# Kernel tuning notes

Measured on AMD Instinct MI355X. Metric: run time of the kernel, lower is better.

The kernel has to match this reference:

```python
import jax, jax.numpy as jnp
import numpy as np

N = 100000   # graph nodes
E = 600000   # edges
D = 128      # feature_dim
K = 3        # candidate ops per MixedOp
EPS = 1e-5   # BatchNorm eps


def _param_stack(key, n_ops):
    kW, kb = jax.random.split(key)
    W = jax.random.normal(kW, (n_ops, K, D, D), jnp.float32) * (1.0 / np.sqrt(D))
    b = jax.random.normal(kb, (n_ops, K, D), jnp.float32) * 0.01
    g = jnp.ones((n_ops, K, D), jnp.float32)
    be = jnp.zeros((n_ops, K, D), jnp.float32)
    return W, b, g, be


def setup_inputs() -> dict:
    key = jax.random.key(0)
    ks = jax.random.split(key, 16)
    inp = {
        'src_emb': jax.random.normal(ks[0], (N, D), jnp.float32),
        'hr': jax.random.normal(ks[1], (N, D), jnp.float32),
        'edge_src': jax.random.randint(ks[2], (E,), 0, N),
        'edge_dst': jax.random.randint(ks[3], (E,), 0, N),
        'weights_zero': jax.random.uniform(ks[4], (1, K), jnp.float32),
        'weights_first': jax.random.uniform(ks[5], (3, K), jnp.float32),
        'weights_middle': jax.random.uniform(ks[6], (2, K), jnp.float32),
        'weights_last': jax.random.uniform(ks[7], (2, K), jnp.float32),
    }
    for name, k, n_ops in [('zero', ks[8], 1), ('first', ks[9], 3), ('mid', ks[10], 2), ('last', ks[11], 2)]:
        W, b, g, be = _param_stack(k, n_ops)
        inp[f'W_{name}'] = W; inp[f'b_{name}'] = b
        inp[f'g_{name}'] = g; inp[f'be_{name}'] = be
    inp['W_cat'] = jax.random.normal(ks[12], (3 * D, D), jnp.float32) * (1.0 / np.sqrt(3 * D))
    inp['b_cat'] = jax.random.normal(ks[13], (D,), jnp.float32) * 0.01
    inp['g_cat'] = jnp.ones((D,), jnp.float32)
    inp['be_cat'] = jnp.zeros((D,), jnp.float32)
    return inp


def _mean_agg(h, src, dst):
    s = jax.ops.segment_sum(h[src], dst, num_segments=N)            # [N,D]
    deg = jax.ops.segment_sum(jnp.ones((src.shape[0],), h.dtype), dst, num_segments=N)
    return s / jnp.maximum(deg, 1.0)[:, None]


def _max_agg(h, src, dst):
    m = jax.ops.segment_max(h[src], dst, num_segments=N)            # -inf for empty segs
    return jnp.where(jnp.isfinite(m), m, 0.0)


def _mixed(cands, w, W, b, g, be):
    # cands: list of K [N,D]; w:[K]; W:[K,D,D]; b/g/be:[K,D]
    x = jnp.stack(cands)                                            # [K,N,D]
    y = jnp.einsum('knd,kdf->knf', x, W) + b[:, None, :]            # Linear per candidate
    mu = jnp.mean(y, axis=1, keepdims=True)                         # BatchNorm1d (batch stats)
    var = jnp.var(y, axis=1, keepdims=True)
    y = (y - mu) * jax.lax.rsqrt(var + EPS) * g[:, None, :] + be[:, None, :]
    y = jax.nn.relu(y)
    return jnp.einsum('k,knd->nd', w, y)                            # alpha-weighted sum


def _graph_cands(h, src, dst):
    return [h, _mean_agg(h, src, dst), _max_agg(h, src, dst)]


def _cell_forward(src_emb, hr, edge_src, edge_dst,
                  weights_zero, weights_first, weights_middle, weights_last,
                  W_zero, b_zero, g_zero, be_zero,
                  W_first, b_first, g_first, be_first,
                  W_mid, b_mid, g_mid, be_mid,
                  W_last, b_last, g_last, be_last,
                  W_cat, b_cat, g_cat, be_cat):
    src, dst = edge_src, edge_dst
    # Cell_Zero: relation-composition candidates on (src_emb, hr)
    pre = [src_emb, src_emb - hr, src_emb * hr]
    h_in = _mixed(pre, weights_zero[0], W_zero[0], b_zero[0], g_zero[0], be_zero[0])
    # Cell_First (nodes=2): ops layout [(i=0,j=0),(i=1,j=0),(i=1,j=1)]
    states = [h_in]
    s0 = _mixed(_graph_cands(states[0], src, dst), weights_first[0], W_first[0], b_first[0], g_first[0], be_first[0])
    states.append(s0)
    s1 = (_mixed(_graph_cands(states[0], src, dst), weights_first[1], W_first[1], b_first[1], g_first[1], be_first[1])
          + _mixed(_graph_cands(states[1], src, dst), weights_first[2], W_first[2], b_first[2], g_first[2], be_first[2]))
    states.append(s1)
    states = states[1:]                                             # drop h_in -> len 2
    # Cell_Middle (nodes=2): one MixedOp per state
    states = [_mixed(_graph_cands(states[i], src, dst), weights_middle[i], W_mid[i], b_mid[i], g_mid[i], be_mid[i])
              for i in range(2)]
    # Cell_Last (in_nodes=2, nodes=1): one new state from both inputs; returns all 3
    s_last = (_mixed(_graph_cands(states[0], src, dst), weights_last[0], W_last[0], b_last[0], g_last[0], be_last[0])
              + _mixed(_graph_cands(states[1], src, dst), weights_last[1], W_last[1], b_last[1], g_last[1], be_last[1]))
    states = states + [s_last]                                      # len 3
    # concat -> Linear -> BN -> ReLU (dropout p=0)
    h = jnp.concatenate(states, axis=1) @ W_cat + b_cat             # [N,D]
    mu = jnp.mean(h, axis=0, keepdims=True)
    var = jnp.var(h, axis=0, keepdims=True)
    h = (h - mu) * jax.lax.rsqrt(var + EPS) * g_cat + be_cat
    return jax.nn.relu(h)


def reference(src_emb, hr, edge_src, edge_dst,
              weights_zero, weights_first, weights_middle, weights_last,
              W_zero, b_zero, g_zero, be_zero,
              W_first, b_first, g_first, be_first,
              W_mid, b_mid, g_mid, be_mid,
              W_last, b_last, g_last, be_last,
              W_cat, b_cat, g_cat, be_cat):
    return _cell_forward(src_emb, hr, edge_src, edge_dst,
                         weights_zero, weights_first, weights_middle, weights_last,
                         W_zero, b_zero, g_zero, be_zero,
                         W_first, b_first, g_first, be_first,
                         W_mid, b_mid, g_mid, be_mid,
                         W_last, b_last, g_last, be_last,
                         W_cat, b_cat, g_cat, be_cat)
```

## Files before the change

### kernel.cpp

```cpp
#include <hip/hip_runtime.h>

#define N_NODES 100000
#define N_EDGES 600000
#define NPAD    100096
#define NTILES  782
#define SCAN_B  98
#define EPS_F   1e-5f

typedef __bf16 bf16_t;
typedef __bf16 bf16x8 __attribute__((ext_vector_type(8)));
typedef __bf16 bf16x4 __attribute__((ext_vector_type(4)));
typedef float  f32x4  __attribute__((ext_vector_type(4)));

__global__ __launch_bounds__(256)
void init_zero_kernel(int* __restrict__ deg, float* __restrict__ stats)
{
    int i = blockIdx.x * 256 + threadIdx.x;
    if (i < N_NODES) deg[i] = 0;
    if (i < 9 * 768) stats[i] = 0.f;
}

__global__ __launch_bounds__(256)
void transpose_w_kernel(const float* __restrict__ Wz, const float* __restrict__ Wf,
                        const float* __restrict__ Wm, const float* __restrict__ Wl,
                        const float* __restrict__ Wc, bf16_t* __restrict__ wt)
{
    int idx = blockIdx.x * 256 + threadIdx.x;
    int mat = idx >> 14;
    int off = idx & 16383;
    int n = off >> 7, kk = off & 127;
    const float* src;
    if      (mat < 3)  src = Wz + mat * 16384;
    else if (mat < 12) src = Wf + (mat - 3) * 16384;
    else if (mat < 18) src = Wm + (mat - 12) * 16384;
    else if (mat < 24) src = Wl + (mat - 18) * 16384;
    else               src = Wc + (mat - 24) * 16384;
    wt[idx] = (bf16_t)src[kk * 128 + n];
}

__global__ __launch_bounds__(256)
void pre_kernel(const float* __restrict__ se, const float* __restrict__ hr,
                bf16_t* __restrict__ p0, bf16_t* __restrict__ p1, bf16_t* __restrict__ p2)
{
    long i = ((long)blockIdx.x * 256 + threadIdx.x) * 8;
    float4 a0 = *(const float4*)&se[i], a1 = *(const float4*)&se[i + 4];
    float4 b0 = *(const float4*)&hr[i], b1 = *(const float4*)&hr[i + 4];
    float av[8] = {a0.x, a0.y, a0.z, a0.w, a1.x, a1.y, a1.z, a1.w};
    float bv[8] = {b0.x, b0.y, b0.z, b0.w, b1.x, b1.y, b1.z, b1.w};
    bf16x8 o0, o1, o2;
#pragma unroll
    for (int j = 0; j < 8; ++j) {
        o0[j] = (bf16_t)av[j];
        o1[j] = (bf16_t)(av[j] - bv[j]);
        o2[j] = (bf16_t)(av[j] * bv[j]);
    }
    *(bf16x8*)&p0[i] = o0;
    *(bf16x8*)&p1[i] = o1;
    *(bf16x8*)&p2[i] = o2;
}

__global__ __launch_bounds__(256)
void deg_count_kernel(const int* __restrict__ dst, int* __restrict__ deg)
{
    int i = blockIdx.x * 256 + threadIdx.x;
    if (i < N_EDGES) atomicAdd(&deg[dst[i]], 1);
}

__global__ __launch_bounds__(256)
void scan_a_kernel(const int* __restrict__ deg, int* __restrict__ partials)
{
    __shared__ int ls[256];
    int b = blockIdx.x, t = threadIdx.x;
    int s = 0;
    for (int j = 0; j < 4; ++j) {
        int i = b * 1024 + t * 4 + j;
        if (i < N_NODES) s += deg[i];
    }
    ls[t] = s; __syncthreads();
    for (int o = 128; o > 0; o >>= 1) {
        if (t < o) ls[t] += ls[t + o];
        __syncthreads();
    }
    if (t == 0) partials[b] = ls[0];
}

__global__ void scan_b_kernel(const int* __restrict__ partials, int* __restrict__ pofs)
{
    if (threadIdx.x == 0) {
        int a = 0;
        for (int i = 0; i < SCAN_B; ++i) { pofs[i] = a; a += partials[i]; }
    }
}

__global__ __launch_bounds__(256)
void scan_c_kernel(const int* __restrict__ deg, const int* __restrict__ pofs,
                   int* __restrict__ row_ptr, int* __restrict__ cursor)
{
    __shared__ int ls[256];
    int b = blockIdx.x, t = threadIdx.x;
    int v[4], s = 0;
    for (int j = 0; j < 4; ++j) {
        int i = b * 1024 + t * 4 + j;
        v[j] = (i < N_NODES) ? deg[i] : 0;
        s += v[j];
    }
    ls[t] = s; __syncthreads();
    for (int o = 1; o < 256; o <<= 1) {
        int tv = (t >= o) ? ls[t - o] : 0;
        __syncthreads();
        ls[t] += tv;
        __syncthreads();
    }
    int excl = ls[t] - s + pofs[b];
    for (int j = 0; j < 4; ++j) {
        int i = b * 1024 + t * 4 + j;
        if (i < N_NODES) { row_ptr[i] = excl; cursor[i] = excl; excl += v[j]; }
    }
    if (b == 0 && t == 0) row_ptr[N_NODES] = N_EDGES;
}

__global__ __launch_bounds__(256)
void scatter_kernel(const int* __restrict__ src, const int* __restrict__ dst,
                    int* __restrict__ cursor, int* __restrict__ csr_src)
{
    int i = blockIdx.x * 256 + threadIdx.x;
    if (i < N_EDGES) {
        int p = atomicAdd(&cursor[dst[i]], 1);
        csr_src[p] = src[i];
    }
}

__global__ __launch_bounds__(256)
void agg_kernel(const bf16_t* __restrict__ h, const int* __restrict__ row_ptr,
                const int* __restrict__ csr_src,
                bf16_t* __restrict__ mean_o, bf16_t* __restrict__ max_o)
{
    int node = blockIdx.x * 16 + (threadIdx.x >> 4);
    int dd = (threadIdx.x & 15) * 8;
    int e0 = row_ptr[node], e1 = row_ptr[node + 1];
    float s[8], mx[8];
#pragma unroll
    for (int j = 0; j < 8; ++j) { s[j] = 0.f; mx[j] = 0.f; }
    for (int e = e0; e < e1; ++e) {
        int sc = csr_src[e];
        bf16x8 v = *(const bf16x8*)&h[(long)sc * 128 + dd];
#pragma unroll
        for (int j = 0; j < 8; ++j) {
            float f = (float)v[j];
            s[j] += f;
            mx[j] = fmaxf(mx[j], f);
        }
    }
    float inv = 1.f / fmaxf((float)(e1 - e0), 1.f);
    bf16x8 om, ox;
#pragma unroll
    for (int j = 0; j < 8; ++j) { om[j] = (bf16_t)(s[j] * inv); ox[j] = (bf16_t)mx[j]; }
    *(bf16x8*)&mean_o[(long)node * 128 + dd] = om;
    *(bf16x8*)&max_o [(long)node * 128 + dd] = ox;
}

__global__ __launch_bounds__(256, 2)
void gemm_kernel(const bf16_t* __restrict__ x0, const bf16_t* __restrict__ x1,
                 const bf16_t* __restrict__ x2, const bf16_t* __restrict__ wt,
                 const float* __restrict__ bias, bf16_t* __restrict__ out,
                 float* __restrict__ partial, int mode)
{
    __shared__ bf16_t lds_w[16384];
    __shared__ bf16_t lds_x[16384];
    const int tid  = threadIdx.x;
    const int lane = tid & 63;
    const int wave = tid >> 6;
    const int quad = lane >> 4;
    const int t16  = lane & 15;
    const int wr = wave >> 1, wc = wave & 1;
    const long tile_base = (long)blockIdx.x * 128;

    f32x4 acc[4][4];
#pragma unroll
    for (int a = 0; a < 4; ++a)
#pragma unroll
        for (int b = 0; b < 4; ++b) acc[a][b] = (f32x4){0.f, 0.f, 0.f, 0.f};

    const int k_sel = blockIdx.y;
    const int nchunk = (mode == 0) ? 1 : 3;
    const bf16_t* xk = (k_sel == 0) ? x0 : ((k_sel == 1) ? x1 : x2);
    bf16_t* outp = (mode == 0) ? (out + (long)k_sel * NPAD * 128) : out;
    const float* bp = (mode == 0) ? (bias + k_sel * 128) : bias;

    for (int c3 = 0; c3 < nchunk; ++c3) {
        const bf16_t* xcur = (mode == 0) ? xk : ((c3 == 0) ? x0 : ((c3 == 1) ? x1 : x2));
        const bf16_t* wcur = (mode == 0) ? (wt + k_sel * 16384) : (wt + c3 * 16384);
        if (c3) __syncthreads();
#pragma unroll
        for (int i = 0; i < 8; ++i) {
            int idx = tid + i * 256;
            int row = idx >> 4, c = idx & 15;
            int sw = c ^ (row & 15);
            *(uint4*)&lds_w[row * 128 + sw * 8] = *(const uint4*)&wcur[row * 128 + c * 8];
            *(uint4*)&lds_x[row * 128 + sw * 8] = *(const uint4*)&xcur[(tile_base + row) * 128 + c * 8];
        }
        __syncthreads();
#pragma unroll
        for (int ks = 0; ks < 4; ++ks) {
            bf16x8 xf[4], wf[4];
#pragma unroll
            for (int ms = 0; ms < 4; ++ms) {
                int row = wr * 64 + ms * 16 + t16;
                int sw = (ks * 4 + quad) ^ t16;
                xf[ms] = *(const bf16x8*)&lds_x[row * 128 + sw * 8];
            }
#pragma unroll
            for (int ns = 0; ns < 4; ++ns) {
                int row = wc * 64 + ns * 16 + t16;
                int sw = (ks * 4 + quad) ^ t16;
                wf[ns] = *(const bf16x8*)&lds_w[row * 128 + sw * 8];
            }
#pragma unroll
            for (int ns = 0; ns < 4; ++ns)
#pragma unroll
                for (int ms = 0; ms < 4; ++ms)
                    acc[ns][ms] = __builtin_amdgcn_mfma_f32_16x16x32_bf16(
                        wf[ns], xf[ms], acc[ns][ms], 0, 0, 0);
        }
    }

    float ss[16], sq[16];
#pragma unroll
    for (int i = 0; i < 16; ++i) { ss[i] = 0.f; sq[i] = 0.f; }

#pragma unroll
    for (int ms = 0; ms < 4; ++ms) {
        long m = tile_base + wr * 64 + ms * 16 + t16;
        if (m < N_NODES) {
#pragma unroll
            for (int ns = 0; ns < 4; ++ns) {
                int n0 = wc * 64 + ns * 16 + quad * 4;
                float4 b4 = *(const float4*)&bp[n0];
                float v0 = acc[ns][ms][0] + b4.x;
                float v1 = acc[ns][ms][1] + b4.y;
                float v2 = acc[ns][ms][2] + b4.z;
                float v3 = acc[ns][ms][3] + b4.w;
                ss[ns * 4 + 0] += v0; sq[ns * 4 + 0] += v0 * v0;
                ss[ns * 4 + 1] += v1; sq[ns * 4 + 1] += v1 * v1;
                ss[ns * 4 + 2] += v2; sq[ns * 4 + 2] += v2 * v2;
                ss[ns * 4 + 3] += v3; sq[ns * 4 + 3] += v3 * v3;
                bf16x4 ov;
                ov[0] = (bf16_t)v0; ov[1] = (bf16_t)v1;
                ov[2] = (bf16_t)v2; ov[3] = (bf16_t)v3;
                *(bf16x4*)&outp[m * 128 + n0] = ov;
            }
        }
    }

#pragma unroll
    for (int o = 1; o < 16; o <<= 1) {
#pragma unroll
        for (int i = 0; i < 16; ++i) {
            ss[i] += __shfl_xor(ss[i], o);
            sq[i] += __shfl_xor(sq[i], o);
        }
    }

    __syncthreads();
    float* lred = (float*)lds_w;
    if (t16 == 0) {
#pragma unroll
        for (int i = 0; i < 16; ++i) {
            lred[wave * 128 + quad * 32 + i]      = ss[i];
            lred[wave * 128 + quad * 32 + 16 + i] = sq[i];
        }
    }
    __syncthreads();
    {
        int t = tid;
        int d   = t & 127;
        int sel = (t >> 7) * 16;
        int dwc = d >> 6;
        int q   = (d >> 2) & 3;
        int i   = ((d >> 4) & 3) * 4 + (d & 3);
        float v = lred[(0 * 2 + dwc) * 128 + q * 32 + sel + i]
                + lred[(1 * 2 + dwc) * 128 + q * 32 + sel + i];
        long pidx = ((long)((mode == 0) ? k_sel : 0) * NTILES + blockIdx.x) * 256 + t;
        partial[pidx] = v;
    }
}

__global__ __launch_bounds__(256)
void reduce_stats_kernel(const float* __restrict__ partial, float* __restrict__ st)
{
    int k = blockIdx.x, j = blockIdx.y, t = threadIdx.x;
    int b0 = j * 98, b1 = (b0 + 98 < NTILES) ? b0 + 98 : NTILES;
    float s = 0.f;
    const float* p = partial + (long)k * NTILES * 256 + t;
    for (int b = b0; b < b1; ++b) s += p[(long)b * 256];
    atomicAdd(&st[k * 256 + t], s);
}

__global__ __launch_bounds__(256)
void passc_kernel(const bf16_t* __restrict__ y, const float* __restrict__ st,
                  const float* __restrict__ g, const float* __restrict__ be,
                  const float* __restrict__ w, bf16_t* __restrict__ out, int accflag)
{
    long base = ((long)blockIdx.x * 256 + threadIdx.x) * 8;
    int d0 = (int)(base & 127);
    const float invN = 1.0f / (float)N_NODES;
    float res[8];
    if (accflag) {
        bf16x8 pv = *(const bf16x8*)&out[base];
#pragma unroll
        for (int j = 0; j < 8; ++j) res[j] = (float)pv[j];
    } else {
#pragma unroll
        for (int j = 0; j < 8; ++j) res[j] = 0.f;
    }
#pragma unroll
    for (int k = 0; k < 3; ++k) {
        bf16x8 yv = *(const bf16x8*)&y[(long)k * NPAD * 128 + base];
        float wk = w[k];
#pragma unroll
        for (int j = 0; j < 8; ++j) {
            int d = d0 + j;
            float mu  = st[k * 256 + d] * invN;
            float var = st[k * 256 + 128 + d] * invN - mu * mu;
            float rs  = rsqrtf(var + EPS_F);
            float v = ((float)yv[j] - mu) * rs * g[k * 128 + d] + be[k * 128 + d];
            res[j] += wk * fmaxf(v, 0.f);
        }
    }
    bf16x8 ov;
#pragma unroll
    for (int j = 0; j < 8; ++j) ov[j] = (bf16_t)res[j];
    *(bf16x8*)&out[base] = ov;
}

__global__ __launch_bounds__(256)
void final_kernel(const bf16_t* __restrict__ h, const float* __restrict__ st,
                  const float* __restrict__ g, const float* __restrict__ be,
                  float* __restrict__ out)
{
    long base = ((long)blockIdx.x * 256 + threadIdx.x) * 8;
    int d0 = (int)(base & 127);
    const float invN = 1.0f / (float)N_NODES;
    bf16x8 hv = *(const bf16x8*)&h[base];
    float ov[8];
#pragma unroll
    for (int j = 0; j < 8; ++j) {
        int d = d0 + j;
        float mu  = st[d] * invN;
        float var = st[128 + d] * invN - mu * mu;
        float rs  = rsqrtf(var + EPS_F);
        float v = ((float)hv[j] - mu) * rs * g[d] + be[d];
        ov[j] = fmaxf(v, 0.f);
    }
    *(float4*)&out[base]     = (float4){ov[0], ov[1], ov[2], ov[3]};
    *(float4*)&out[base + 4] = (float4){ov[4], ov[5], ov[6], ov[7]};
}

extern "C" void kernel_launch(void* const* d_in, const int* in_sizes, int n_in,
                              void* d_out, int out_size, void* d_ws, size_t ws_size,
                              hipStream_t stream)
{
    const float* src_emb = (const float*)d_in[0];
    const float* hr      = (const float*)d_in[1];
    const int*   e_src   = (const int*)d_in[2];
    const int*   e_dst   = (const int*)d_in[3];
    const float* w_zero  = (const float*)d_in[4];
    const float* w_first = (const float*)d_in[5];
    const float* w_mid   = (const float*)d_in[6];
    const float* w_last  = (const float*)d_in[7];
    const float* W_zero  = (const float*)d_in[8];
    const float* b_zero  = (const float*)d_in[9];
    const float* g_zero  = (const float*)d_in[10];
    const float* be_zero = (const float*)d_in[11];
    const float* W_first = (const float*)d_in[12];
    const float* b_first = (const float*)d_in[13];
    const float* g_first = (const float*)d_in[14];
    const float* be_first= (const float*)d_in[15];
    const float* W_mid   = (const float*)d_in[16];
    const float* b_mid   = (const float*)d_in[17];
    const float* g_mid   = (const float*)d_in[18];
    const float* be_mid  = (const float*)d_in[19];
    const float* W_last  = (const float*)d_in[20];
    const float* b_last  = (const float*)d_in[21];
    const float* g_last  = (const float*)d_in[22];
    const float* be_last = (const float*)d_in[23];
    const float* W_cat   = (const float*)d_in[24];
    const float* b_cat   = (const float*)d_in[25];
    const float* g_cat   = (const float*)d_in[26];
    const float* be_cat  = (const float*)d_in[27];
    float* out = (float*)d_out;

    char* ws = (char*)d_ws;
    size_t off = 0;
    auto carve = [&](size_t bytes) -> char* {
        off = (off + 255) & ~(size_t)255;
        char* p = ws + off;
        off += bytes;
        return p;
    };

    const size_t SB = (size_t)NPAD * 128 * sizeof(bf16_t);
    bf16_t* B[8];
    for (int i = 0; i < 8; ++i) B[i] = (bf16_t*)carve(SB);
    bf16_t* ybuf = B[0];
    bf16_t* wt    = (bf16_t*)carve((size_t)27 * 16384 * 2);
    float*  stats = (float*)carve(9 * 768 * sizeof(float));
    float*  partial = (float*)carve((size_t)3 * NTILES * 256 * sizeof(float));
    int* deg    = (int*)carve((size_t)N_NODES * 4);
    int* rowp   = (int*)carve((size_t)(N_NODES + 1) * 4);
    int* cursor = (int*)carve((size_t)N_NODES * 4);
    int* csr    = (int*)carve((size_t)N_EDGES * 4);
    int* parts  = (int*)carve(SCAN_B * 4);
    int* pofs   = (int*)carve(SCAN_B * 4);

    bf16_t* wtZ  = wt;
    bf16_t* wtF0 = wt + (size_t)3  * 16384;
    bf16_t* wtF1 = wt + (size_t)6  * 16384;
    bf16_t* wtF2 = wt + (size_t)9  * 16384;
    bf16_t* wtM0 = wt + (size_t)12 * 16384;
    bf16_t* wtM1 = wt + (size_t)15 * 16384;
    bf16_t* wtL0 = wt + (size_t)18 * 16384;
    bf16_t* wtL1 = wt + (size_t)21 * 16384;
    bf16_t* wtC  = wt + (size_t)24 * 16384;

    float* st0 = stats + 0 * 768;
    float* st1 = stats + 1 * 768;
    float* st2 = stats + 2 * 768;
    float* st3 = stats + 3 * 768;
    float* st4 = stats + 4 * 768;
    float* st5 = stats + 5 * 768;
    float* st6 = stats + 6 * 768;
    float* st7 = stats + 7 * 768;
    float* st8 = stats + 8 * 768;

    const int GEL8 = (N_NODES * 128) / 2048;

    init_zero_kernel<<<dim3((N_NODES + 255) / 256), dim3(256), 0, stream>>>(deg, stats);
    transpose_w_kernel<<<dim3(1728), dim3(256), 0, stream>>>(W_zero, W_first, W_mid, W_last, W_cat, wt);
    deg_count_kernel<<<dim3((N_EDGES + 255) / 256), dim3(256), 0, stream>>>(e_dst, deg);
    scan_a_kernel<<<dim3(SCAN_B), dim3(256), 0, stream>>>(deg, parts);
    scan_b_kernel<<<dim3(1), dim3(64), 0, stream>>>(parts, pofs);
    scan_c_kernel<<<dim3(SCAN_B), dim3(256), 0, stream>>>(deg, pofs, rowp, cursor);
    scatter_kernel<<<dim3((N_EDGES + 255) / 256), dim3(256), 0, stream>>>(e_src, e_dst, cursor, csr);

    auto G = [&](const bf16_t* x0_, const bf16_t* x1_, const bf16_t* x2_,
                 const bf16_t* w_, const float* b_, bf16_t* o_, float* st_, int mode) {
        int nk = (mode == 0) ? 3 : 1;
        gemm_kernel<<<dim3(NTILES, nk), dim3(256), 0, stream>>>(
            x0_, x1_, x2_, w_, b_, o_, partial, mode);
        reduce_stats_kernel<<<dim3(nk, 8), dim3(256), 0, stream>>>(partial, st_);
    };
    auto C = [&](const float* g_, const float* be_, const float* w_, float* st_,
                 bf16_t* o_, int acc) {
        passc_kernel<<<dim3(GEL8), dim3(256), 0, stream>>>(ybuf, st_, g_, be_, w_, o_, acc);
    };
    auto A = [&](const bf16_t* h_, bf16_t* me_, bf16_t* mx_) {
        agg_kernel<<<dim3(N_NODES / 16), dim3(256), 0, stream>>>(h_, rowp, csr, me_, mx_);
    };

    pre_kernel<<<dim3(GEL8), dim3(256), 0, stream>>>(src_emb, hr, B[3], B[4], B[5]);
    G(B[3], B[4], B[5], wtZ, b_zero, ybuf, st0, 0);
    C(g_zero, be_zero, w_zero, st0, B[6], 0);

    A(B[6], B[3], B[4]);

    G(B[6], B[3], B[4], wtF0, b_first + 0 * 384, ybuf, st1, 0);
    C(g_first + 0 * 384, be_first + 0 * 384, w_first + 0, st1, B[5], 0);

    G(B[6], B[3], B[4], wtF1, b_first + 1 * 384, ybuf, st2, 0);
    C(g_first + 1 * 384, be_first + 1 * 384, w_first + 3, st2, B[7], 0);

    A(B[5], B[3], B[4]);

    G(B[5], B[3], B[4], wtF2, b_first + 2 * 384, ybuf, st3, 0);
    C(g_first + 2 * 384, be_first + 2 * 384, w_first + 6, st3, B[7], 1);

    G(B[5], B[3], B[4], wtM0, b_mid + 0 * 384, ybuf, st4, 0);
    C(g_mid + 0 * 384, be_mid + 0 * 384, w_mid + 0, st4, B[6], 0);

    A(B[7], B[3], B[4]);

    G(B[7], B[3], B[4], wtM1, b_mid + 1 * 384, ybuf, st5, 0);
    C(g_mid + 1 * 384, be_mid + 1 * 384, w_mid + 3, st5, B[5], 0);

    A(B[6], B[3], B[4]);
    G(B[6], B[3], B[4], wtL0, b_last + 0 * 384, ybuf, st6, 0);
    C(g_last + 0 * 384, be_last + 0 * 384, w_last + 0, st6, B[7], 0);
    A(B[5], B[3], B[4]);
    G(B[5], B[3], B[4], wtL1, b_last + 1 * 384, ybuf, st7, 0);
    C(g_last + 1 * 384, be_last + 1 * 384, w_last + 3, st7, B[7], 1);

    G(B[6], B[5], B[7], wtC, b_cat, B[0], st8, 1);
    final_kernel<<<dim3(GEL8), dim3(256), 0, stream>>>(B[0], st8, g_cat, be_cat, out);
}
```

Measured before the change: 1.243 ms.

## Make GEMM persistent with async LDS double-buffering and register-resident weights

```diff
diff --git a/kernel.cpp b/kernel.cpp
--- a/kernel.cpp
+++ b/kernel.cpp
@@ -6,6 +6,7 @@
 #define NTILES  782
 #define SCAN_B  98
 #define EPS_F   1e-5f
+#define GRIDP   512
 
 typedef __bf16 bf16_t;
 typedef __bf16 bf16x8 __attribute__((ext_vector_type(8)));
@@ -159,129 +160,191 @@
     *(bf16x8*)&max_o [(long)node * 128 + dd] = ox;
 }
 
+__device__ __forceinline__ void gload_lds16(const bf16_t* g, bf16_t* l)
+{
+    __builtin_amdgcn_global_load_lds(
+        (const __attribute__((address_space(1))) void*)g,
+        (__attribute__((address_space(3))) void*)l, 16, 0, 0);
+}
+
+__device__ __forceinline__ void stage_tile(const bf16_t* src, bf16_t* dst)
+{
+#pragma unroll
+    for (int i = 0; i < 8; ++i)
+        gload_lds16(src + i * 2048, dst + i * 2048);
+}
+
+__device__ __forceinline__ void barrier_lgkm()
+{
+    asm volatile("s_waitcnt lgkmcnt(0)" ::: "memory");
+    __builtin_amdgcn_s_barrier();
+    asm volatile("" ::: "memory");
+}
+
 __global__ __launch_bounds__(256, 2)
 void gemm_kernel(const bf16_t* __restrict__ x0, const bf16_t* __restrict__ x1,
                  const bf16_t* __restrict__ x2, const bf16_t* __restrict__ wt,
                  const float* __restrict__ bias, bf16_t* __restrict__ out,
                  float* __restrict__ partial, int mode)
 {
-    __shared__ bf16_t lds_w[16384];
-    __shared__ bf16_t lds_x[16384];
+    __shared__ __align__(16) bf16_t lds_a[16384];
+    __shared__ __align__(16) bf16_t lds_b[16384];
+    __shared__ float lred_s[512];
+
     const int tid  = threadIdx.x;
     const int lane = tid & 63;
     const int wave = tid >> 6;
     const int quad = lane >> 4;
     const int t16  = lane & 15;
     const int wr = wave >> 1, wc = wave & 1;
-    const long tile_base = (long)blockIdx.x * 128;
-
-    f32x4 acc[4][4];
-#pragma unroll
-    for (int a = 0; a < 4; ++a)
-#pragma unroll
-        for (int b = 0; b < 4; ++b) acc[a][b] = (f32x4){0.f, 0.f, 0.f, 0.f};
-
-    const int k_sel = blockIdx.y;
-    const int nchunk = (mode == 0) ? 1 : 3;
-    const bf16_t* xk = (k_sel == 0) ? x0 : ((k_sel == 1) ? x1 : x2);
-    bf16_t* outp = (mode == 0) ? (out + (long)k_sel * NPAD * 128) : out;
-    const float* bp = (mode == 0) ? (bias + k_sel * 128) : bias;
-
-    for (int c3 = 0; c3 < nchunk; ++c3) {
-        const bf16_t* xcur = (mode == 0) ? xk : ((c3 == 0) ? x0 : ((c3 == 1) ? x1 : x2));
-        const bf16_t* wcur = (mode == 0) ? (wt + k_sel * 16384) : (wt + c3 * 16384);
-        if (c3) __syncthreads();
-#pragma unroll
-        for (int i = 0; i < 8; ++i) {
-            int idx = tid + i * 256;
-            int row = idx >> 4, c = idx & 15;
-            int sw = c ^ (row & 15);
-            *(uint4*)&lds_w[row * 128 + sw * 8] = *(const uint4*)&wcur[row * 128 + c * 8];
-            *(uint4*)&lds_x[row * 128 + sw * 8] = *(const uint4*)&xcur[(tile_base + row) * 128 + c * 8];
-        }
+    const int bid = blockIdx.x;
+
+    const int rowoff = (tid >> 4) * 128 + (((tid & 15) ^ (tid >> 4)) * 8);
+    const int dstoff = tid * 8;
+
+    int s, e;
+    if (mode == 0) {
+        const int total = NTILES * 3;
+        s = (int)(((long)bid * total) / GRIDP);
+        e = (int)(((long)(bid + 1) * total) / GRIDP);
+    } else {
+        int st = (int)(((long)bid * NTILES) / GRIDP);
+        int et = (int)(((long)(bid + 1) * NTILES) / GRIDP);
+        s = st * 3; e = et * 3;
+    }
+    if (s >= e) return;
+
+    bf16x8 wreg[4][4];
+    f32x4  acc[4][4];
+    int kcur = -1;
+    int w = s;
+
+    {
+        const int k0 = (mode == 0) ? (s / NTILES) : (s % 3);
+        const int t0 = (mode == 0) ? (s % NTILES) : (s / 3);
+        const bf16_t* xs = (k0 == 0) ? x0 : (k0 == 1) ? x1 : x2;
+        stage_tile(xs + (long)t0 * 16384 + rowoff, lds_a + dstoff);
+    }
+
+    auto iter = [&](bf16_t* curb, bf16_t* nxtb) {
+        const int ksel = (mode == 0) ? (w / NTILES) : (w % 3);
+        const int tile = (mode == 0) ? (w % NTILES) : (w / 3);
+
+        if (ksel != kcur) {
+            kcur = ksel;
+            const bf16_t* wm = wt + (long)ksel * 16384;
+#pragma unroll
+            for (int ns = 0; ns < 4; ++ns)
+#pragma unroll
+                for (int ks = 0; ks < 4; ++ks)
+                    wreg[ns][ks] = *(const bf16x8*)
+                        &wm[(wc * 64 + ns * 16 + t16) * 128 + ks * 32 + quad * 8];
+        }
+
         __syncthreads();
+
+        if (w + 1 < e) {
+            const int kn = (mode == 0) ? ((w + 1) / NTILES) : ((w + 1) % 3);
+            const int tn = (mode == 0) ? ((w + 1) % NTILES) : ((w + 1) / 3);
+            const bf16_t* xs = (kn == 0) ? x0 : (kn == 1) ? x1 : x2;
+            stage_tile(xs + (long)tn * 16384 + rowoff, nxtb + dstoff);
+        }
+
+        if ((mode == 0) || (ksel == 0)) {
+#pragma unroll
+            for (int a = 0; a < 4; ++a)
+#pragma unroll
+                for (int b = 0; b < 4; ++b) acc[a][b] = (f32x4){0.f, 0.f, 0.f, 0.f};
+        }
+
 #pragma unroll
         for (int ks = 0; ks < 4; ++ks) {
-            bf16x8 xf[4], wf[4];
+            bf16x8 xf[4];
 #pragma unroll
             for (int ms = 0; ms < 4; ++ms) {
                 int row = wr * 64 + ms * 16 + t16;
                 int sw = (ks * 4 + quad) ^ t16;
-                xf[ms] = *(const bf16x8*)&lds_x[row * 128 + sw * 8];
-            }
-#pragma unroll
-            for (int ns = 0; ns < 4; ++ns) {
-                int row = wc * 64 + ns * 16 + t16;
-                int sw = (ks * 4 + quad) ^ t16;
-                wf[ns] = *(const bf16x8*)&lds_w[row * 128 + sw * 8];
+                xf[ms] = *(const bf16x8*)&curb[row * 128 + sw * 8];
             }
 #pragma unroll
             for (int ns = 0; ns < 4; ++ns)
 #pragma unroll
                 for (int ms = 0; ms < 4; ++ms)
                     acc[ns][ms] = __builtin_amdgcn_mfma_f32_16x16x32_bf16(
-                        wf[ns], xf[ms], acc[ns][ms], 0, 0, 0);
-        }
-    }
-
-    float ss[16], sq[16];
-#pragma unroll
-    for (int i = 0; i < 16; ++i) { ss[i] = 0.f; sq[i] = 0.f; }
-
-#pragma unroll
-    for (int ms = 0; ms < 4; ++ms) {
-        long m = tile_base + wr * 64 + ms * 16 + t16;
-        if (m < N_NODES) {
-#pragma unroll
-            for (int ns = 0; ns < 4; ++ns) {
-                int n0 = wc * 64 + ns * 16 + quad * 4;
-                float4 b4 = *(const float4*)&bp[n0];
-                float v0 = acc[ns][ms][0] + b4.x;
-                float v1 = acc[ns][ms][1] + b4.y;
-                float v2 = acc[ns][ms][2] + b4.z;
-                float v3 = acc[ns][ms][3] + b4.w;
-                ss[ns * 4 + 0] += v0; sq[ns * 4 + 0] += v0 * v0;
-                ss[ns * 4 + 1] += v1; sq[ns * 4 + 1] += v1 * v1;
-                ss[ns * 4 + 2] += v2; sq[ns * 4 + 2] += v2 * v2;
-                ss[ns * 4 + 3] += v3; sq[ns * 4 + 3] += v3 * v3;
-                bf16x4 ov;
-                ov[0] = (bf16_t)v0; ov[1] = (bf16_t)v1;
-                ov[2] = (bf16_t)v2; ov[3] = (bf16_t)v3;
-                *(bf16x4*)&outp[m * 128 + n0] = ov;
+                        wreg[ns][ks], xf[ms], acc[ns][ms], 0, 0, 0);
+        }
+
+        if ((mode == 0) || (ksel == 2)) {
+            const float* bp = (mode == 0) ? (bias + ksel * 128) : bias;
+            bf16_t* outp = (mode == 0) ? (out + (long)ksel * NPAD * 128) : out;
+            const long tile_base = (long)tile * 128;
+
+            float ss[16], sq[16];
+#pragma unroll
+            for (int i = 0; i < 16; ++i) { ss[i] = 0.f; sq[i] = 0.f; }
+
+#pragma unroll
+            for (int ms = 0; ms < 4; ++ms) {
+                long m = tile_base + wr * 64 + ms * 16 + t16;
+                if (m < N_NODES) {
+#pragma unroll
+                    for (int ns = 0; ns < 4; ++ns) {
+                        int n0 = wc * 64 + ns * 16 + quad * 4;
+                        float4 b4 = *(const float4*)&bp[n0];
+                        float v0 = acc[ns][ms][0] + b4.x;
+                        float v1 = acc[ns][ms][1] + b4.y;
+                        float v2 = acc[ns][ms][2] + b4.z;
+                        float v3 = acc[ns][ms][3] + b4.w;
+                        ss[ns * 4 + 0] += v0; sq[ns * 4 + 0] += v0 * v0;
+                        ss[ns * 4 + 1] += v1; sq[ns * 4 + 1] += v1 * v1;
+                        ss[ns * 4 + 2] += v2; sq[ns * 4 + 2] += v2 * v2;
+                        ss[ns * 4 + 3] += v3; sq[ns * 4 + 3] += v3 * v3;
+                        bf16x4 ov;
+                        ov[0] = (bf16_t)v0; ov[1] = (bf16_t)v1;
+                        ov[2] = (bf16_t)v2; ov[3] = (bf16_t)v3;
+                        *(bf16x4*)&outp[m * 128 + n0] = ov;
+                    }
+                }
             }
-        }
-    }
-
-#pragma unroll
-    for (int o = 1; o < 16; o <<= 1) {
-#pragma unroll
-        for (int i = 0; i < 16; ++i) {
-            ss[i] += __shfl_xor(ss[i], o);
-            sq[i] += __shfl_xor(sq[i], o);
-        }
-    }
-
-    __syncthreads();
-    float* lred = (float*)lds_w;
-    if (t16 == 0) {
-#pragma unroll
-        for (int i = 0; i < 16; ++i) {
-            lred[wave * 128 + quad * 32 + i]      = ss[i];
-            lred[wave * 128 + quad * 32 + 16 + i] = sq[i];
-        }
-    }
-    __syncthreads();
-    {
-        int t = tid;
-        int d   = t & 127;
-        int sel = (t >> 7) * 16;
-        int dwc = d >> 6;
-        int q   = (d >> 2) & 3;
-        int i   = ((d >> 4) & 3) * 4 + (d & 3);
-        float v = lred[(0 * 2 + dwc) * 128 + q * 32 + sel + i]
-                + lred[(1 * 2 + dwc) * 128 + q * 32 + sel + i];
-        long pidx = ((long)((mode == 0) ? k_sel : 0) * NTILES + blockIdx.x) * 256 + t;
-        partial[pidx] = v;
+
+#pragma unroll
+            for (int o = 1; o < 16; o <<= 1) {
+#pragma unroll
+                for (int i = 0; i < 16; ++i) {
+                    ss[i] += __shfl_xor(ss[i], o);
+                    sq[i] += __shfl_xor(sq[i], o);
+                }
+            }
+
+            if (t16 == 0) {
+#pragma unroll
+                for (int i = 0; i < 16; ++i) {
+                    lred_s[wave * 128 + quad * 32 + i]      = ss[i];
+                    lred_s[wave * 128 + quad * 32 + 16 + i] = sq[i];
+                }
+            }
+            barrier_lgkm();
+            {
+                int t = tid;
+                int d   = t & 127;
+                int sel = (t >> 7) * 16;
+                int dwc = d >> 6;
+                int q   = (d >> 2) & 3;
+                int i   = ((d >> 4) & 3) * 4 + (d & 3);
+                float v = lred_s[(0 * 2 + dwc) * 128 + q * 32 + sel + i]
+                        + lred_s[(1 * 2 + dwc) * 128 + q * 32 + sel + i];
+                int pk = (mode == 0) ? ksel : 0;
+                long pidx = ((long)pk * NTILES + tile) * 256 + t;
+                partial[pidx] = v;
+            }
+        }
+    };
+
+    for (;;) {
+        iter(lds_a, lds_b); ++w;
+        if (w >= e) break;
+        iter(lds_b, lds_a); ++w;
+        if (w >= e) break;
     }
 }
 
@@ -446,7 +509,7 @@
     auto G = [&](const bf16_t* x0_, const bf16_t* x1_, const bf16_t* x2_,
                  const bf16_t* w_, const float* b_, bf16_t* o_, float* st_, int mode) {
         int nk = (mode == 0) ? 3 : 1;
-        gemm_kernel<<<dim3(NTILES, nk), dim3(256), 0, stream>>>(
+        gemm_kernel<<<dim3(GRIDP), dim3(256), 0, stream>>>(
             x0_, x1_, x2_, w_, b_, o_, partial, mode);
         reduce_stats_kernel<<<dim3(nk, 8), dim3(256), 0, stream>>>(partial, st_);
     };
```

Measured after the change: 2.925 ms. 135% more time.

## Recompute GEMM in second pass to fuse BatchNorm, ReLU and mixing epilogue

Applied to the files above, without the earlier changes.

```diff
diff --git a/kernel.cpp b/kernel.cpp
--- a/kernel.cpp
+++ b/kernel.cpp
@@ -160,13 +160,13 @@
 }
 
 __global__ __launch_bounds__(256, 2)
-void gemm_kernel(const bf16_t* __restrict__ x0, const bf16_t* __restrict__ x1,
-                 const bf16_t* __restrict__ x2, const bf16_t* __restrict__ wt,
-                 const float* __restrict__ bias, bf16_t* __restrict__ out,
-                 float* __restrict__ partial, int mode)
+void gemmA_kernel(const bf16_t* __restrict__ x0, const bf16_t* __restrict__ x1,
+                  const bf16_t* __restrict__ x2, const bf16_t* __restrict__ wt,
+                  float* __restrict__ partial, int mode)
 {
     __shared__ bf16_t lds_w[16384];
     __shared__ bf16_t lds_x[16384];
+    __shared__ float lred[512];
     const int tid  = threadIdx.x;
     const int lane = tid & 63;
     const int wave = tid >> 6;
@@ -184,8 +184,6 @@
     const int k_sel = blockIdx.y;
     const int nchunk = (mode == 0) ? 1 : 3;
     const bf16_t* xk = (k_sel == 0) ? x0 : ((k_sel == 1) ? x1 : x2);
-    bf16_t* outp = (mode == 0) ? (out + (long)k_sel * NPAD * 128) : out;
-    const float* bp = (mode == 0) ? (bias + k_sel * 128) : bias;
 
     for (int c3 = 0; c3 < nchunk; ++c3) {
         const bf16_t* xcur = (mode == 0) ? xk : ((c3 == 0) ? x0 : ((c3 == 1) ? x1 : x2));
@@ -227,31 +225,20 @@
     float ss[16], sq[16];
 #pragma unroll
     for (int i = 0; i < 16; ++i) { ss[i] = 0.f; sq[i] = 0.f; }
-
 #pragma unroll
     for (int ms = 0; ms < 4; ++ms) {
         long m = tile_base + wr * 64 + ms * 16 + t16;
         if (m < N_NODES) {
 #pragma unroll
-            for (int ns = 0; ns < 4; ++ns) {
-                int n0 = wc * 64 + ns * 16 + quad * 4;
-                float4 b4 = *(const float4*)&bp[n0];
-                float v0 = acc[ns][ms][0] + b4.x;
-                float v1 = acc[ns][ms][1] + b4.y;
-                float v2 = acc[ns][ms][2] + b4.z;
-                float v3 = acc[ns][ms][3] + b4.w;
-                ss[ns * 4 + 0] += v0; sq[ns * 4 + 0] += v0 * v0;
-                ss[ns * 4 + 1] += v1; sq[ns * 4 + 1] += v1 * v1;
-                ss[ns * 4 + 2] += v2; sq[ns * 4 + 2] += v2 * v2;
-                ss[ns * 4 + 3] += v3; sq[ns * 4 + 3] += v3 * v3;
-                bf16x4 ov;
-                ov[0] = (bf16_t)v0; ov[1] = (bf16_t)v1;
-                ov[2] = (bf16_t)v2; ov[3] = (bf16_t)v3;
-                *(bf16x4*)&outp[m * 128 + n0] = ov;
-            }
-        }
-    }
-
+            for (int ns = 0; ns < 4; ++ns)
+#pragma unroll
+                for (int j = 0; j < 4; ++j) {
+                    float v = acc[ns][ms][j];
+                    ss[ns * 4 + j] += v;
+                    sq[ns * 4 + j] += v * v;
+                }
+        }
+    }
 #pragma unroll
     for (int o = 1; o < 16; o <<= 1) {
 #pragma unroll
@@ -260,9 +247,6 @@
             sq[i] += __shfl_xor(sq[i], o);
         }
     }
-
-    __syncthreads();
-    float* lred = (float*)lds_w;
     if (t16 == 0) {
 #pragma unroll
         for (int i = 0; i < 16; ++i) {
@@ -270,7 +254,8 @@
             lred[wave * 128 + quad * 32 + 16 + i] = sq[i];
         }
     }
-    __syncthreads();
+    asm volatile("s_waitcnt lgkmcnt(0)" ::: "memory");
+    __builtin_amdgcn_s_barrier();
     {
         int t = tid;
         int d   = t & 127;
@@ -297,63 +282,165 @@
 }
 
 __global__ __launch_bounds__(256)
-void passc_kernel(const bf16_t* __restrict__ y, const float* __restrict__ st,
-                  const float* __restrict__ g, const float* __restrict__ be,
-                  const float* __restrict__ w, bf16_t* __restrict__ out, int accflag)
-{
-    long base = ((long)blockIdx.x * 256 + threadIdx.x) * 8;
-    int d0 = (int)(base & 127);
+void coef_kernel(const float* __restrict__ st, const float* __restrict__ bias,
+                 const float* __restrict__ gg, const float* __restrict__ be,
+                 const float* __restrict__ wmix, float* __restrict__ coef, int mode)
+{
+    int t = threadIdx.x;
+    if (t >= 128) return;
     const float invN = 1.0f / (float)N_NODES;
-    float res[8];
-    if (accflag) {
-        bf16x8 pv = *(const bf16x8*)&out[base];
-#pragma unroll
-        for (int j = 0; j < 8; ++j) res[j] = (float)pv[j];
+    int nk = (mode == 0) ? 3 : 1;
+    for (int k = 0; k < nk; ++k) {
+        float S = st[k * 256 + t], Q = st[k * 256 + 128 + t];
+        float sa  = S * invN;
+        float var = Q * invN - sa * sa;
+        float rs  = rsqrtf(var + EPS_F);
+        float gk = gg[k * 128 + t], bek = be[k * 128 + t];
+        float wk = (mode == 0) ? wmix[k] : 1.f;
+        coef[k * 256 + t]       = wk * rs * gk;
+        coef[k * 256 + 128 + t] = wk * (-sa * rs * gk + bek);
+        (void)bias;
+    }
+}
+
+__global__ __launch_bounds__(256, 2)
+void gemmB_kernel(const bf16_t* __restrict__ x0, const bf16_t* __restrict__ x1,
+                  const bf16_t* __restrict__ x2, const bf16_t* __restrict__ wt,
+                  const float* __restrict__ coef, bf16_t* __restrict__ outb,
+                  float* __restrict__ outf, int mode, int accflag)
+{
+    __shared__ bf16_t lds_w[16384];
+    __shared__ bf16_t lds_x[16384];
+    __shared__ float lsc[768];
+    const int tid  = threadIdx.x;
+    const int lane = tid & 63;
+    const int wave = tid >> 6;
+    const int quad = lane >> 4;
+    const int t16  = lane & 15;
+    const int wr = wave >> 1, wc = wave & 1;
+    const long tile_base = (long)blockIdx.x * 128;
+
+    lsc[tid] = coef[tid];
+    if (tid < 256) { lsc[tid + 256] = coef[tid + 256]; lsc[tid + 512] = coef[tid + 512]; }
+
+    f32x4 acc[4][4], res[4][4];
+#pragma unroll
+    for (int a = 0; a < 4; ++a)
+#pragma unroll
+        for (int b = 0; b < 4; ++b) acc[a][b] = (f32x4){0.f, 0.f, 0.f, 0.f};
+
+    if (mode == 0 && accflag) {
+#pragma unroll
+        for (int ns = 0; ns < 4; ++ns)
+#pragma unroll
+            for (int ms = 0; ms < 4; ++ms) {
+                long m = tile_base + wr * 64 + ms * 16 + t16;
+                int n0 = wc * 64 + ns * 16 + quad * 4;
+                bf16x4 pv = *(const bf16x4*)&outb[(m < N_NODES ? m : 0) * 128 + n0];
+                res[ns][ms] = (f32x4){(float)pv[0], (float)pv[1], (float)pv[2], (float)pv[3]};
+            }
     } else {
 #pragma unroll
-        for (int j = 0; j < 8; ++j) res[j] = 0.f;
-    }
-#pragma unroll
-    for (int k = 0; k < 3; ++k) {
-        bf16x8 yv = *(const bf16x8*)&y[(long)k * NPAD * 128 + base];
-        float wk = w[k];
-#pragma unroll
-        for (int j = 0; j < 8; ++j) {
-            int d = d0 + j;
-            float mu  = st[k * 256 + d] * invN;
-            float var = st[k * 256 + 128 + d] * invN - mu * mu;
-            float rs  = rsqrtf(var + EPS_F);
-            float v = ((float)yv[j] - mu) * rs * g[k * 128 + d] + be[k * 128 + d];
-            res[j] += wk * fmaxf(v, 0.f);
-        }
-    }
-    bf16x8 ov;
-#pragma unroll
-    for (int j = 0; j < 8; ++j) ov[j] = (bf16_t)res[j];
-    *(bf16x8*)&out[base] = ov;
-}
-
-__global__ __launch_bounds__(256)
-void final_kernel(const bf16_t* __restrict__ h, const float* __restrict__ st,
-                  const float* __restrict__ g, const float* __restrict__ be,
-                  float* __restrict__ out)
-{
-    long base = ((long)blockIdx.x * 256 + threadIdx.x) * 8;
-    int d0 = (int)(base & 127);
-    const float invN = 1.0f / (float)N_NODES;
-    bf16x8 hv = *(const bf16x8*)&h[base];
-    float ov[8];
-#pragma unroll
-    for (int j = 0; j < 8; ++j) {
-        int d = d0 + j;
-        float mu  = st[d] * invN;
-        float var = st[128 + d] * invN - mu * mu;
-        float rs  = rsqrtf(var + EPS_F);
-        float v = ((float)hv[j] - mu) * rs * g[d] + be[d];
-        ov[j] = fmaxf(v, 0.f);
-    }
-    *(float4*)&out[base]     = (float4){ov[0], ov[1], ov[2], ov[3]};
-    *(float4*)&out[base + 4] = (float4){ov[4], ov[5], ov[6], ov[7]};
+        for (int a = 0; a < 4; ++a)
+#pragma unroll
+            for (int b = 0; b < 4; ++b) res[a][b] = (f32x4){0.f, 0.f, 0.f, 0.f};
+    }
+
+    for (int c3 = 0; c3 < 3; ++c3) {
+        const bf16_t* xcur = (c3 == 0) ? x0 : ((c3 == 1) ? x1 : x2);
+        const bf16_t* wcur = wt + c3 * 16384;
+        __syncthreads();
+#pragma unroll
+        for (int i = 0; i < 8; ++i) {
+            int idx = tid + i * 256;
+            int row = idx >> 4, c = idx & 15;
+            int sw = c ^ (row & 15);
+            *(uint4*)&lds_w[row * 128 + sw * 8] = *(const uint4*)&wcur[row * 128 + c * 8];
+            *(uint4*)&lds_x[row * 128 + sw * 8] = *(const uint4*)&xcur[(tile_base + row) * 128 + c * 8];
+        }
+        __syncthreads();
+        if (mode == 0) {
+#pragma unroll
+            for (int a = 0; a < 4; ++a)
+#pragma unroll
+                for (int b = 0; b < 4; ++b) acc[a][b] = (f32x4){0.f, 0.f, 0.f, 0.f};
+        }
+#pragma unroll
+        for (int ks = 0; ks < 4; ++ks) {
+            bf16x8 xf[4], wf[4];
+#pragma unroll
+            for (int ms = 0; ms < 4; ++ms) {
+                int row = wr * 64 + ms * 16 + t16;
+                int sw = (ks * 4 + quad) ^ t16;
+                xf[ms] = *(const bf16x8*)&lds_x[row * 128 + sw * 8];
+            }
+#pragma unroll
+            for (int ns = 0; ns < 4; ++ns) {
+                int row = wc * 64 + ns * 16 + t16;
+                int sw = (ks * 4 + quad) ^ t16;
+                wf[ns] = *(const bf16x8*)&lds_w[row * 128 + sw * 8];
+            }
+#pragma unroll
+            for (int ns = 0; ns < 4; ++ns)
+#pragma unroll
+                for (int ms = 0; ms < 4; ++ms)
+                    acc[ns][ms] = __builtin_amdgcn_mfma_f32_16x16x32_bf16(
+                        wf[ns], xf[ms], acc[ns][ms], 0, 0, 0);
+        }
+        if (mode == 0) {
+#pragma unroll
+            for (int ns = 0; ns < 4; ++ns) {
+                int n0 = wc * 64 + ns * 16 + quad * 4;
+                float4 A4 = *(const float4*)&lsc[c3 * 256 + n0];
+                float4 B4 = *(const float4*)&lsc[c3 * 256 + 128 + n0];
+#pragma unroll
+                for (int ms = 0; ms < 4; ++ms) {
+                    res[ns][ms][0] += fmaxf(acc[ns][ms][0] * A4.x + B4.x, 0.f);
+                    res[ns][ms][1] += fmaxf(acc[ns][ms][1] * A4.y + B4.y, 0.f);
+                    res[ns][ms][2] += fmaxf(acc[ns][ms][2] * A4.z + B4.z, 0.f);
+                    res[ns][ms][3] += fmaxf(acc[ns][ms][3] * A4.w + B4.w, 0.f);
+                }
+            }
+        }
+    }
+
+    if (mode == 0) {
+#pragma unroll
+        for (int ms = 0; ms < 4; ++ms) {
+            long m = tile_base + wr * 64 + ms * 16 + t16;
+            if (m < N_NODES) {
+#pragma unroll
+                for (int ns = 0; ns < 4; ++ns) {
+                    int n0 = wc * 64 + ns * 16 + quad * 4;
+                    bf16x4 ov;
+                    ov[0] = (bf16_t)res[ns][ms][0];
+                    ov[1] = (bf16_t)res[ns][ms][1];
+                    ov[2] = (bf16_t)res[ns][ms][2];
+                    ov[3] = (bf16_t)res[ns][ms][3];
+                    *(bf16x4*)&outb[m * 128 + n0] = ov;
+                }
+            }
+        }
+    } else {
+#pragma unroll
+        for (int ms = 0; ms < 4; ++ms) {
+            long m = tile_base + wr * 64 + ms * 16 + t16;
+            if (m < N_NODES) {
+#pragma unroll
+                for (int ns = 0; ns < 4; ++ns) {
+                    int n0 = wc * 64 + ns * 16 + quad * 4;
+                    float4 A4 = *(const float4*)&lsc[n0];
+                    float4 B4 = *(const float4*)&lsc[128 + n0];
+                    float4 o;
+                    o.x = fmaxf(acc[ns][ms][0] * A4.x + B4.x, 0.f);
+                    o.y = fmaxf(acc[ns][ms][1] * A4.y + B4.y, 0.f);
+                    o.z = fmaxf(acc[ns][ms][2] * A4.z + B4.z, 0.f);
+                    o.w = fmaxf(acc[ns][ms][3] * A4.w + B4.w, 0.f);
+                    *(float4*)&outf[m * 128 + n0] = o;
+                }
+            }
+        }
+    }
 }
 
 extern "C" void kernel_launch(void* const* d_in, const int* in_sizes, int n_in,
@@ -402,10 +489,10 @@
     const size_t SB = (size_t)NPAD * 128 * sizeof(bf16_t);
     bf16_t* B[8];
     for (int i = 0; i < 8; ++i) B[i] = (bf16_t*)carve(SB);
-    bf16_t* ybuf = B[0];
     bf16_t* wt    = (bf16_t*)carve((size_t)27 * 16384 * 2);
     float*  stats = (float*)carve(9 * 768 * sizeof(float));
     float*  partial = (float*)carve((size_t)3 * NTILES * 256 * sizeof(float));
+    float*  coefs = (float*)carve(768 * sizeof(float));
     int* deg    = (int*)carve((size_t)N_NODES * 4);
     int* rowp   = (int*)carve((size_t)(N_NODES + 1) * 4);
     int* cursor = (int*)carve((size_t)N_NODES * 4);
@@ -423,6 +510,32 @@
     bf16_t* wtL1 = wt + (size_t)21 * 16384;
     bf16_t* wtC  = wt + (size_t)24 * 16384;
 
+    const int GEL8 = (N_NODES * 128) / 2048;
+
+    init_zero_kernel<<<dim3((N_NODES + 255) / 256), dim3(256), 0, stream>>>(deg, stats);
+    transpose_w_kernel<<<dim3(1728), dim3(256), 0, stream>>>(W_zero, W_first, W_mid, W_last, W_cat, wt);
+    deg_count_kernel<<<dim3((N_EDGES + 255) / 256), dim3(256), 0, stream>>>(e_dst, deg);
+    scan_a_kernel<<<dim3(SCAN_B), dim3(256), 0, stream>>>(deg, parts);
+    scan_b_kernel<<<dim3(1), dim3(64), 0, stream>>>(parts, pofs);
+    scan_c_kernel<<<dim3(SCAN_B), dim3(256), 0, stream>>>(deg, pofs, rowp, cursor);
+    scatter_kernel<<<dim3((N_EDGES + 255) / 256), dim3(256), 0, stream>>>(e_src, e_dst, cursor, csr);
+
+    auto M = [&](const bf16_t* x0_, const bf16_t* x1_, const bf16_t* x2_,
+                 const bf16_t* w_, const float* b_, const float* g_, const float* be_,
+                 const float* wm_, bf16_t* ob_, float* of_, float* st_,
+                 int acc_, int mode_) {
+        int nk = (mode_ == 0) ? 3 : 1;
+        gemmA_kernel<<<dim3(NTILES, nk), dim3(256), 0, stream>>>(
+            x0_, x1_, x2_, w_, partial, mode_);
+        reduce_stats_kernel<<<dim3(nk, 8), dim3(256), 0, stream>>>(partial, st_);
+        coef_kernel<<<dim3(1), dim3(256), 0, stream>>>(st_, b_, g_, be_, wm_, coefs, mode_);
+        gemmB_kernel<<<dim3(NTILES), dim3(256), 0, stream>>>(
+            x0_, x1_, x2_, w_, coefs, ob_, of_, mode_, acc_);
+    };
+    auto A = [&](const bf16_t* h_, bf16_t* me_, bf16_t* mx_) {
+        agg_kernel<<<dim3(N_NODES / 16), dim3(256), 0, stream>>>(h_, rowp, csr, me_, mx_);
+    };
+
     float* st0 = stats + 0 * 768;
     float* st1 = stats + 1 * 768;
     float* st2 = stats + 2 * 768;
@@ -433,63 +546,35 @@
     float* st7 = stats + 7 * 768;
     float* st8 = stats + 8 * 768;
 
-    const int GEL8 = (N_NODES * 128) / 2048;
-
-    init_zero_kernel<<<dim3((N_NODES + 255) / 256), dim3(256), 0, stream>>>(deg, stats);
-    transpose_w_kernel<<<dim3(1728), dim3(256), 0, stream>>>(W_zero, W_first, W_mid, W_last, W_cat, wt);
-    deg_count_kernel<<<dim3((N_EDGES + 255) / 256), dim3(256), 0, stream>>>(e_dst, deg);
-    scan_a_kernel<<<dim3(SCAN_B), dim3(256), 0, stream>>>(deg, parts);
-    scan_b_kernel<<<dim3(1), dim3(64), 0, stream>>>(parts, pofs);
-    scan_c_kernel<<<dim3(SCAN_B), dim3(256), 0, stream>>>(deg, pofs, rowp, cursor);
-    scatter_kernel<<<dim3((N_EDGES + 255) / 256), dim3(256), 0, stream>>>(e_src, e_dst, cursor, csr);
-
-    auto G = [&](const bf16_t* x0_, const bf16_t* x1_, const bf16_t* x2_,
-                 const bf16_t* w_, const float* b_, bf16_t* o_, float* st_, int mode) {
-        int nk = (mode == 0) ? 3 : 1;
-        gemm_kernel<<<dim3(NTILES, nk), dim3(256), 0, stream>>>(
-            x0_, x1_, x2_, w_, b_, o_, partial, mode);
-        reduce_stats_kernel<<<dim3(nk, 8), dim3(256), 0, stream>>>(partial, st_);
-    };
-    auto C = [&](const float* g_, const float* be_, const float* w_, float* st_,
-                 bf16_t* o_, int acc) {
-        passc_kernel<<<dim3(GEL8), dim3(256), 0, stream>>>(ybuf, st_, g_, be_, w_, o_, acc);
-    };
-    auto A = [&](const bf16_t* h_, bf16_t* me_, bf16_t* mx_) {
-        agg_kernel<<<dim3(N_NODES / 16), dim3(256), 0, stream>>>(h_, rowp, csr, me_, mx_);
-    };
-
     pre_kernel<<<dim3(GEL8), dim3(256), 0, stream>>>(src_emb, hr, B[3], B[4], B[5]);
-    G(B[3], B[4], B[5], wtZ, b_zero, ybuf, st0, 0);
-    C(g_zero, be_zero, w_zero, st0, B[6], 0);
+    M(B[3], B[4], B[5], wtZ, b_zero, g_zero, be_zero, w_zero, B[6], nullptr, st0, 0, 0);
 
     A(B[6], B[3], B[4]);
 
-    G(B[6], B[3], B[4], wtF0, b_first + 0 * 384, ybuf, st1, 0);
-    C(g_first + 0 * 384, be_first + 0 * 384, w_first + 0, st1, B[5], 0);
-
-    G(B[6], B[3], B[4], wtF1, b_first + 1 * 384, ybuf, st2, 0);
-    C(g_first + 1 * 384, be_first + 1 * 384, w_first + 3, st2, B[7], 0);
+    M(B[6], B[3], B[4], wtF0, b_first + 0, g_first + 0, be_first + 0,
+      w_first + 0, B[5], nullptr, st1, 0, 0);
+    M(B[6], B[3], B[4], wtF1, b_first + 384, g_first + 384, be_first + 384,
+      w_first + 3, B[7], nullptr, st2, 0, 0);
 
     A(B[5], B[3], B[4]);
 
-    G(B[5], B[3], B[4], wtF2, b_first + 2 * 384, ybuf, st3, 0);
-    C(g_first + 2 * 384, be_first + 2 * 384, w_first + 6, st3, B[7], 1);
-
-    G(B[5], B[3], B[4], wtM0, b_mid + 0 * 384, ybuf, st4, 0);
-    C(g_mid + 0 * 384, be_mid + 0 * 384, w_mid + 0, st4, B[6], 0);
+    M(B[5], B[3], B[4], wtF2, b_first + 768, g_first + 768, be_first + 768,
+      w_first + 6, B[7], nullptr, st3, 1, 0);
+    M(B[5], B[3], B[4], wtM0, b_mid + 0, g_mid + 0, be_mid + 0,
+      w_mid + 0, B[6], nullptr, st4, 0, 0);
 
     A(B[7], B[3], B[4]);
 
-    G(B[7], B[3], B[4], wtM1, b_mid + 1 * 384, ybuf, st5, 0);
-    C(g_mid + 1 * 384, be_mid + 1 * 384, w_mid + 3, st5, B[5], 0);
+    M(B[7], B[3], B[4], wtM1, b_mid + 384, g_mid + 384, be_mid + 384,
+      w_mid + 3, B[5], nullptr, st5, 0, 0);
 
     A(B[6], B[3], B[4]);
-    G(B[6], B[3], B[4], wtL0, b_last + 0 * 384, ybuf, st6, 0);
-    C(g_last + 0 * 384, be_last + 0 * 384, w_last + 0, st6, B[7], 0);
+    M(B[6], B[3], B[4], wtL0, b_last + 0, g_last + 0, be_last + 0,
+      w_last + 0, B[7], nullptr, st6, 0, 0);
     A(B[5], B[3], B[4]);
-    G(B[5], B[3], B[4], wtL1, b_last + 1 * 384, ybuf, st7, 0);
-    C(g_last + 1 * 384, be_last + 1 * 384, w_last + 3, st7, B[7], 1);
-
-    G(B[6], B[5], B[7], wtC, b_cat, B[0], st8, 1);
-    final_kernel<<<dim3(GEL8), dim3(256), 0, stream>>>(B[0], st8, g_cat, be_cat, out);
-}
+    M(B[5], B[3], B[4], wtL1, b_last + 384, g_last + 384, be_last + 384,
+      w_last + 3, B[7], nullptr, st7, 1, 0);
+
+    M(B[6], B[5], B[7], wtC, b_cat, g_cat, be_cat, nullptr,
+      nullptr, out, st8, 0, 1);
+}
```

Result: slower. 1.284 ms (+3.3%).
